# Kernel optimization log

Hardware: AMD Instinct MI355X
Metric: run time of the kernel (lower is better)

Reference implementation:

```python
import jax, jax.numpy as jnp
import numpy as np

B, N, C = 32, 1025, 768
H, D = 12, 64          # num_heads, head_dim
M = 4 * D              # num random features = 256
HEIGHT, WIDTH = 32, 32 # spatial grid; N = HEIGHT*WIDTH + 1 (CLS)
EPS = 1e-6


def setup_inputs() -> dict:
    key = jax.random.key(0)
    ks = jax.random.split(key, 7)
    x = jax.random.normal(ks[0], (B, N, C), jnp.float32)
    w_qkv = jax.random.normal(ks[1], (3 * C, C), jnp.float32) * 0.02
    w_proj = jax.random.normal(ks[2], (C, C), jnp.float32) * 0.02
    b_proj = jnp.zeros((C,), jnp.float32)
    c_row = jax.random.normal(ks[3], (H, D), jnp.float32) * 0.02
    c_col = jax.random.normal(ks[4], (H, D), jnp.float32) * 0.02
    # orthogonal random-feature projection (m, d): QR blocks scaled by chi norm
    blocks = []
    for i in range(M // D):
        Hm = jax.random.normal(jax.random.fold_in(ks[5], i), (D, D), jnp.float32)
        Q, _ = jnp.linalg.qr(Hm)
        nrm = jnp.linalg.norm(jax.random.normal(jax.random.fold_in(ks[6], i), (D,), jnp.float32))
        blocks.append(Q * nrm)
    proj_feat = jnp.concatenate(blocks, axis=0)  # (M, D)
    return {"x": x, "w_qkv": w_qkv, "w_proj": w_proj, "b_proj": b_proj,
            "c_row": c_row, "c_col": c_col, "proj_feat": proj_feat}


def _string(xp, c_row, c_col):
    """Circulant-STRING rotation. xp: (B,H,Np,D)."""
    rows = jnp.arange(HEIGHT, dtype=jnp.float32)
    cols = jnp.arange(WIDTH, dtype=jnp.float32)
    gr, gc = jnp.meshgrid(rows, cols, indexing='ij')
    pos_r = gr.ravel()  # (Np,)
    pos_c = gc.ravel()
    # g: (H, Np, D)
    g = pos_r[None, :, None] * c_row[:, None, :] + pos_c[None, :, None] * c_col[:, None, :]
    g_fft = jnp.fft.fft(g, axis=-1)
    exp_lambda = jnp.exp(2j * g_fft.imag)          # (H, Np, D) complex, unit modulus
    x_fft = jnp.fft.fft(xp, axis=-1)               # (B, H, Np, D) complex
    rotated = jnp.fft.ifft(exp_lambda[None] * x_fft, axis=-1).real
    return rotated.astype(xp.dtype)


def _favor(x, proj):
    """Positive random feature map. x: (B,H,N,D), proj: (M,D) -> (B,H,N,M)."""
    xs = x * (D ** -0.25)
    px = jnp.einsum('bhnd,md->bhnm', xs, proj)
    norm_sq = 0.5 * jnp.sum(xs * xs, axis=-1, keepdims=True)
    return jnp.exp(px - norm_sq)


def reference(x, w_qkv, w_proj, b_proj, c_row, c_col, proj_feat):
    qkv = x @ w_qkv.T                                  # (B, N, 3C)
    qkv = qkv.reshape(B, N, 3, H, D).transpose(2, 0, 3, 1, 4)  # (3,B,H,N,D)
    q, k, v = qkv[0], qkv[1], qkv[2]
    # N == HEIGHT*WIDTH + 1 -> CLS token at position 0 is left unrotated
    q_cls, q_p = q[:, :, :1, :], q[:, :, 1:, :]
    k_cls, k_p = k[:, :, :1, :], k[:, :, 1:, :]
    q = jnp.concatenate([q_cls, _string(q_p, c_row, c_col)], axis=2)
    k = jnp.concatenate([k_cls, _string(k_p, c_row, c_col)], axis=2)
    q_feat = _favor(q, proj_feat)                      # (B,H,N,M)
    k_feat = _favor(k, proj_feat)
    # bidirectional linear attention
    context = jnp.einsum('bhnm,bhne->bhme', k_feat, v) # (B,H,M,D)
    num = jnp.einsum('bhnm,bhme->bhne', q_feat, context)
    k_sum = k_feat.sum(axis=2)                         # (B,H,M)
    den = jnp.einsum('bhnm,bhm->bhn', q_feat, k_sum)[..., None]
    den = jnp.maximum(den, EPS)
    out = num / den                                    # (B,H,N,D)
    out = out.transpose(0, 2, 1, 3).reshape(B, N, C)
    return out @ w_proj.T + b_proj
```

## Files before the change

### kernel.cpp

```cpp
#include <hip/hip_runtime.h>
#include <math.h>

typedef _Float16 f16;
typedef _Float16 f16x8 __attribute__((ext_vector_type(8)));
typedef _Float16 f16x4 __attribute__((ext_vector_type(4)));
typedef float f32x4 __attribute__((ext_vector_type(4)));

#define LDSK 40
#define NTOK 1025
#define CC 768
#define HH 12
#define DD 64
#define MM 256
#define VPAD 1056
#define BN_ROWS 32800

__device__ __forceinline__ void load_row16(const f16* p, f16x8& a0, f16x8& a1) {
    a0 = *(const f16x8*)p;
    a1 = *(const f16x8*)(p + 8);
}
__device__ __forceinline__ void load_row16(const float* p, f16x8& a0, f16x8& a1) {
    const float4* q = (const float4*)p;
    float4 u0 = q[0], u1 = q[1], u2 = q[2], u3 = q[3];
    a0[0] = (f16)u0.x; a0[1] = (f16)u0.y; a0[2] = (f16)u0.z; a0[3] = (f16)u0.w;
    a0[4] = (f16)u1.x; a0[5] = (f16)u1.y; a0[6] = (f16)u1.z; a0[7] = (f16)u1.w;
    a1[0] = (f16)u2.x; a1[1] = (f16)u2.y; a1[2] = (f16)u2.z; a1[3] = (f16)u2.w;
    a1[4] = (f16)u3.x; a1[5] = (f16)u3.y; a1[6] = (f16)u3.z; a1[7] = (f16)u3.w;
}

__device__ __forceinline__ void gload16(const f16* g, f16* l) {
    __builtin_amdgcn_global_load_lds(
        (const __attribute__((address_space(1))) unsigned int*)g,
        (__attribute__((address_space(3))) unsigned int*)l, 16, 0, 0);
}

__global__ void k_diag(float* out, float v) {
    if (threadIdx.x == 0 && blockIdx.x == 0) out[0] = v;
}

__global__ __launch_bounds__(256) void k_cvt_x(const float* __restrict__ x, f16* __restrict__ xw) {
    size_t i = ((size_t)blockIdx.x * 256 + threadIdx.x) * 4;
    float4 v;
    if (i < (size_t)BN_ROWS * CC) v = *(const float4*)(x + i);
    else v = make_float4(0.f, 0.f, 0.f, 0.f);
    f16x4 o; o[0] = (f16)v.x; o[1] = (f16)v.y; o[2] = (f16)v.z; o[3] = (f16)v.w;
    *(f16x4*)(xw + i) = o;
}

__global__ __launch_bounds__(256) void k_cvt(const float* __restrict__ in, f16* __restrict__ out,
                                             long n, float scale) {
    long i = (long)blockIdx.x * 256 + threadIdx.x;
    if (i < n) out[i] = (f16)(in[i] * scale);
}

__global__ __launch_bounds__(256) void k_zpad(f16* __restrict__ v16t) {
    int bh = blockIdx.x;
    for (int u = threadIdx.x; u < 64 * 31; u += 256) {
        int d = u / 31, j = u - d * 31;
        v16t[((size_t)bh * DD + d) * VPAD + 1025 + j] = (f16)0.f;
    }
}

__global__ __launch_bounds__(64) void k_ab(const float* __restrict__ c_row,
                                           const float* __restrict__ c_col,
                                           float* __restrict__ ab) {
    int h = blockIdx.x, k = threadIdx.x;
    float sa = 0.f, sb = 0.f;
    for (int d = 0; d < 64; ++d) {
        float s = sinf((float)((k * d) & 63) * (6.283185307179586f / 64.f));
        sa += c_row[h * 64 + d] * s;
        sb += c_col[h * 64 + d] * s;
    }
    ab[h * 64 + k] = -2.f * sa;
    ab[768 + h * 64 + k] = -2.f * sb;
}

__global__ __launch_bounds__(64) void k_wcirc(const float* __restrict__ ab, float* __restrict__ wc) {
    int hp = blockIdx.x; int h = hp >> 10; int p = hp & 1023;
    float pr = (float)(p >> 5), pc = (float)(p & 31);
    int t = threadIdx.x;
    __shared__ float th[64];
    th[t] = pr * ab[h * 64 + t] + pc * ab[768 + h * 64 + t];
    __syncthreads();
    float s = 0.f;
    #pragma unroll 8
    for (int k = 0; k < 64; ++k) {
        float arg = th[k] + (float)((k * t) & 63) * (6.283185307179586f / 64.f);
        s += __cosf(arg);
    }
    wc[(size_t)hp * 64 + t] = s * (1.f / 64.f);
}

template <bool GA, typename TA, typename TB>
__device__ __forceinline__ void gemm128_core(const TA* __restrict__ A, const TB* __restrict__ Bm,
                                             int K, int row0, int col0, int Alim,
                                             f32x4 (&acc)[4][4],
                                             f16 (*As)[LDSK], f16 (*Bs)[LDSK]) {
    const int tid = threadIdx.x;
    const int lane = tid & 63;
    const int lr = tid >> 1, lk = (tid & 1) * 16;
    const int frow = lane & 15, fk = (lane >> 4) * 8;
    const int wave = tid >> 6, wr = wave >> 1, wc = wave & 1;
    for (int kt = 0; kt < K; kt += 32) {
        f16x8 a0 = {}, a1 = {}, b0, b1;
        if (!GA || (row0 + lr) < Alim)
            load_row16(A + (size_t)(row0 + lr) * K + kt + lk, a0, a1);
        load_row16(Bm + (size_t)(col0 + lr) * K + kt + lk, b0, b1);
        __syncthreads();
        *(f16x8*)&As[lr][lk] = a0; *(f16x8*)&As[lr][lk + 8] = a1;
        *(f16x8*)&Bs[lr][lk] = b0; *(f16x8*)&Bs[lr][lk + 8] = b1;
        __syncthreads();
        f16x8 af[4], bf[4];
        #pragma unroll
        for (int m = 0; m < 4; ++m) af[m] = *(const f16x8*)&As[wr * 64 + m * 16 + frow][fk];
        #pragma unroll
        for (int n = 0; n < 4; ++n) bf[n] = *(const f16x8*)&Bs[wc * 64 + n * 16 + frow][fk];
        #pragma unroll
        for (int m = 0; m < 4; ++m)
            #pragma unroll
            for (int n = 0; n < 4; ++n)
                acc[m][n] = __builtin_amdgcn_mfma_f32_16x16x32_f16(af[m], bf[n], acc[m][n], 0, 0, 0);
    }
}

__device__ __forceinline__ void gemm256_pipe(const f16* __restrict__ A, const f16* __restrict__ Bm,
                                             int row0, int col0, int aclamp,
                                             f32x4 (&acc)[8][4], f16* As, f16* Bs) {
    const int tid = threadIdx.x;
    const int lane = tid & 63, w = tid >> 6;
    const int frow = lane & 15;
    const int srow = lane >> 3;
    const int schk = ((lane & 7) ^ srow) * 8;
    const f16* aG[4]; const f16* bG[4];
    f16* aL[4]; f16* bL[4];
    #pragma unroll
    for (int j = 0; j < 4; ++j) {
        int ra = row0 + w * 32 + 8 * j + srow;
        if (ra > aclamp) ra = aclamp;
        aG[j] = A + (size_t)ra * CC + schk;
        bG[j] = Bm + (size_t)(col0 + w * 32 + 8 * j + srow) * CC + schk;
        aL[j] = As + (w * 32 + 8 * j) * 64;
        bL[j] = Bs + (w * 32 + 8 * j) * 64;
    }
    auto STAGE = [&](int tt) {
        int bo = (tt & 1) * 16384, ko = tt * 64;
        #pragma unroll
        for (int j = 0; j < 4; ++j) {
            gload16(aG[j] + ko, aL[j] + bo);
            gload16(bG[j] + ko, bL[j] + bo);
        }
    };
    STAGE(0);
    const int wr = w >> 2, wcn = w & 3;
    const int fk8 = (lane >> 4) * 8;
    const int cswz = (frow & 7) * 8;
    for (int t = 0; t < 12; ++t) {
        asm volatile("s_waitcnt vmcnt(0)" ::: "memory");
        __builtin_amdgcn_s_barrier();
        __builtin_amdgcn_sched_barrier(0);
        if (t < 11) STAGE(t + 1);
        const f16* Ac = As + (t & 1) * 16384;
        const f16* Bc = Bs + (t & 1) * 16384;
        #pragma unroll
        for (int ks = 0; ks < 2; ++ks) {
            const int co = (ks * 32 + fk8) ^ cswz;
            f16x8 af[8], bf[4];
            #pragma unroll
            for (int n = 0; n < 4; ++n)
                bf[n] = *(const f16x8*)&Bc[(wcn * 64 + n * 16 + frow) * 64 + co];
            #pragma unroll
            for (int m = 0; m < 8; ++m)
                af[m] = *(const f16x8*)&Ac[(wr * 128 + m * 16 + frow) * 64 + co];
            #pragma unroll
            for (int n = 0; n < 4; ++n)
                #pragma unroll
                for (int m = 0; m < 8; ++m)
                    acc[m][n] = __builtin_amdgcn_mfma_f32_16x16x32_f16(af[m], bf[n], acc[m][n], 0, 0, 0);
        }
    }
}

__global__ __launch_bounds__(512, 2) void k_gemm_qkv_256(const f16* __restrict__ A, const f16* __restrict__ Bm,
                                                         f16* __restrict__ q16, f16* __restrict__ k16,
                                                         f16* __restrict__ v16t) {
    __shared__ __attribute__((aligned(16))) f16 As[2 * 256 * 64];
    __shared__ __attribute__((aligned(16))) f16 Bs[2 * 256 * 64];
    const int q = 145, r = 1;
    int xg = blockIdx.x & 7, o8 = blockIdx.x >> 3;
    int wg = (xg < r ? xg * (q + 1) : r * (q + 1) + (xg - r) * q) + o8;
    int row0 = (wg / 9) * 256, col0 = (wg % 9) * 256;
    f32x4 acc[8][4] = {};
    gemm256_pipe(A, Bm, row0, col0, 32895, acc, As, Bs);
    const int lane = threadIdx.x & 63, w = threadIdx.x >> 6;
    const int wr = w >> 2, wcn = w & 3;
    int cb = col0 + wcn * 64 + (lane & 15);
    int tt = cb / CC;
    int h = (cb - tt * CC) >> 6;
    int d0 = lane & 15;
    int rb = row0 + wr * 128 + 4 * (lane >> 4);
    #pragma unroll
    for (int m = 0; m < 8; ++m)
        #pragma unroll
        for (int i = 0; i < 4; ++i) {
            int rr = rb + m * 16 + i;
            if (rr >= BN_ROWS) continue;
            int b = rr / NTOK, nn = rr - b * NTOK;
            size_t bh = (size_t)b * HH + h;
            if (tt == 0) {
                f16* p = q16 + (bh * NTOK + nn) * DD + d0;
                #pragma unroll
                for (int n = 0; n < 4; ++n) p[n * 16] = (f16)acc[m][n][i];
            } else if (tt == 1) {
                f16* p = k16 + (bh * NTOK + nn) * DD + d0;
                #pragma unroll
                for (int n = 0; n < 4; ++n) p[n * 16] = (f16)acc[m][n][i];
            } else {
                f16* p = v16t + (bh * DD + d0) * VPAD + nn;
                #pragma unroll
                for (int n = 0; n < 4; ++n) p[(size_t)n * 16 * VPAD] = (f16)acc[m][n][i];
            }
        }
}

__global__ __launch_bounds__(512, 2) void k_gemm_proj_256(const f16* __restrict__ A, const f16* __restrict__ Bm,
                                                          const float* __restrict__ bias, float* __restrict__ out) {
    __shared__ __attribute__((aligned(16))) f16 As[2 * 256 * 64];
    __shared__ __attribute__((aligned(16))) f16 Bs[2 * 256 * 64];
    const int q = 48, r = 3;
    int xg = blockIdx.x & 7, o8 = blockIdx.x >> 3;
    int wg = (xg < r ? xg * (q + 1) : r * (q + 1) + (xg - r) * q) + o8;
    int row0 = (wg / 3) * 256, col0 = (wg % 3) * 256;
    f32x4 acc[8][4] = {};
    gemm256_pipe(A, Bm, row0, col0, 32799, acc, As, Bs);
    const int lane = threadIdx.x & 63, w = threadIdx.x >> 6;
    const int wr = w >> 2, wcn = w & 3;
    int cb = col0 + wcn * 64 + (lane & 15);
    float bj[4];
    #pragma unroll
    for (int n = 0; n < 4; ++n) bj[n] = bias[cb + n * 16];
    int rb = row0 + wr * 128 + 4 * (lane >> 4);
    #pragma unroll
    for (int m = 0; m < 8; ++m)
        #pragma unroll
        for (int i = 0; i < 4; ++i) {
            int rr = rb + m * 16 + i;
            if (rr >= BN_ROWS) continue;
            float* p = out + (size_t)rr * CC + cb;
            #pragma unroll
            for (int n = 0; n < 4; ++n) p[n * 16] = acc[m][n][i] + bj[n];
        }
}

__device__ __forceinline__ void qkv_epilogue(f32x4 (&acc)[4][4], int row0, int col0,
                                             f16* __restrict__ q16, f16* __restrict__ k16,
                                             f16* __restrict__ v16t) {
    int lane = threadIdx.x & 63, wave = threadIdx.x >> 6;
    int wr = wave >> 1, wc = wave & 1;
    int rb = row0 + wr * 64 + 4 * (lane >> 4);
    int cb = col0 + wc * 64 + (lane & 15);
    #pragma unroll
    for (int m = 0; m < 4; ++m)
        #pragma unroll
        for (int n = 0; n < 4; ++n)
            #pragma unroll
            for (int i = 0; i < 4; ++i) {
                int r = rb + m * 16 + i;
                if (r >= BN_ROWS) continue;
                int j = cb + n * 16;
                int b = r / NTOK, nn = r - b * NTOK;
                int t = j / CC, rem = j - t * CC;
                int h = rem >> 6, d = rem & 63;
                size_t bh = (size_t)b * HH + h;
                f16 val = (f16)acc[m][n][i];
                if (t == 0) q16[(bh * NTOK + nn) * DD + d] = val;
                else if (t == 1) k16[(bh * NTOK + nn) * DD + d] = val;
                else v16t[(bh * DD + d) * VPAD + nn] = val;
            }
}

__global__ __launch_bounds__(256) void k_gemm_qkv_f32(const float* __restrict__ A, const f16* __restrict__ Bm,
                                                      f16* __restrict__ q16, f16* __restrict__ k16,
                                                      f16* __restrict__ v16t) {
    __shared__ __attribute__((aligned(16))) f16 As[128][LDSK];
    __shared__ __attribute__((aligned(16))) f16 Bs[128][LDSK];
    f32x4 acc[4][4] = {};
    int row0 = blockIdx.x * 128, col0 = blockIdx.y * 128;
    gemm128_core<true>(A, Bm, CC, row0, col0, BN_ROWS, acc, As, Bs);
    qkv_epilogue(acc, row0, col0, q16, k16, v16t);
}

__global__ __launch_bounds__(256) void k_rotate(const float* __restrict__ wcirc,
                                                f16* __restrict__ q16, f16* __restrict__ k16,
                                                float* __restrict__ nsqq, float* __restrict__ nsqk) {
    const int p = blockIdx.x, h = blockIdx.y;
    const int nn = p + 1;
    const int tid = threadIdx.x;
    __shared__ float wl[64];
    __shared__ __attribute__((aligned(16))) f16 Ws[64][72];
    __shared__ __attribute__((aligned(16))) f16 Xs[64][72];
    if (tid < 64) wl[tid] = wcirc[((size_t)h * 1024 + p) * 64 + tid];
    {
        const int row = tid >> 2;
        const int ch = (tid & 3) * 16;
        const int b = row & 31;
        const f16* src = ((row < 32) ? q16 : k16) + (((size_t)b * HH + h) * NTOK + nn) * DD + ch;
        f16x8 v0 = *(const f16x8*)src;
        f16x8 v1 = *(const f16x8*)(src + 8);
        *(f16x8*)&Xs[row][ch] = v0;
        *(f16x8*)&Xs[row][ch + 8] = v1;
    }
    __syncthreads();
    #pragma unroll
    for (int j = 0; j < 16; ++j) {
        int idx = tid * 16 + j;
        int d = idx >> 6, m = idx & 63;
        Ws[d][m] = (f16)wl[(d - m) & 63];
    }
    __syncthreads();
    const int lane = tid & 63, wave = tid >> 6;
    const int frow = lane & 15, fk = (lane >> 4) * 8;
    f32x4 acc[4] = {};
    #pragma unroll
    for (int kt = 0; kt < 64; kt += 32) {
        f16x8 a = *(const f16x8*)&Xs[wave * 16 + frow][kt + fk];
        #pragma unroll
        for (int n = 0; n < 4; ++n) {
            f16x8 bfr = *(const f16x8*)&Ws[n * 16 + frow][kt + fk];
            acc[n] = __builtin_amdgcn_mfma_f32_16x16x32_f16(a, bfr, acc[n], 0, 0, 0);
        }
    }
    #pragma unroll
    for (int i = 0; i < 4; ++i) {
        int row = wave * 16 + 4 * (lane >> 4) + i;
        int b = row & 31;
        f16* dst = ((row < 32) ? q16 : k16) + (((size_t)b * HH + h) * NTOK + nn) * DD;
        float ss = 0.f;
        #pragma unroll
        for (int n = 0; n < 4; ++n) {
            float v = acc[n][i];
            dst[n * 16 + (lane & 15)] = (f16)v;
            ss += v * v;
        }
        ss += __shfl_xor(ss, 1); ss += __shfl_xor(ss, 2);
        ss += __shfl_xor(ss, 4); ss += __shfl_xor(ss, 8);
        if ((lane & 15) == 0) {
            float* nd = (row < 32) ? nsqq : nsqk;
            nd[((size_t)b * HH + h) * NTOK + nn] = ss * (1.f / 16.f);
        }
    }
}

__global__ __launch_bounds__(256) void k_cls_nsq(const f16* __restrict__ q16, const f16* __restrict__ k16,
                                                 float* __restrict__ nsqq, float* __restrict__ nsqk) {
    int gw = (blockIdx.x * 256 + threadIdx.x) >> 6;
    int lane = threadIdx.x & 63;
    int which = gw & 1; int bh = gw >> 1;
    const f16* src = (which ? k16 : q16) + (size_t)bh * NTOK * DD;
    float v = (float)src[lane];
    float ss = v * v;
    for (int off = 1; off < 64; off <<= 1) ss += __shfl_xor(ss, off);
    if (lane == 0) (which ? nsqk : nsqq)[(size_t)bh * NTOK] = ss * (1.f / 16.f);
}

__global__ __launch_bounds__(512) void k_fctx(const f16* __restrict__ k16, const f16* __restrict__ v16t,
                                              const f16* __restrict__ pfeat, const float* __restrict__ nsqk,
                                              f16* __restrict__ ctxT) {
    __shared__ __attribute__((aligned(16))) f16 uLDS[80 * 136];
    f16 (*fts)[LDSK] = (f16(*)[LDSK])uLDS;
    f16 (*cx)[136]   = (f16(*)[136])uLDS;
    const int bh = blockIdx.x;
    const int tid = threadIdx.x;
    const int lane = tid & 63, w = tid >> 6;
    const int frow = lane & 15, fk8 = (lane >> 4) * 8;
    const int m0 = w * 32;
    f16x8 pf[2][2];
    #pragma unroll
    for (int mf = 0; mf < 2; ++mf)
        #pragma unroll
        for (int kf = 0; kf < 2; ++kf)
            pf[mf][kf] = *(const f16x8*)&pfeat[(m0 + mf * 16 + frow) * DD + kf * 32 + fk8];
    const f16* kb_base = k16 + (size_t)bh * NTOK * DD;
    const f16* vb_base = v16t + (size_t)bh * DD * VPAD;
    const float* ns_base = nsqk + (size_t)bh * NTOK;
    auto loadK = [&](f16x8 (&kb)[2][2], int n0) {
        #pragma unroll
        for (int nf = 0; nf < 2; ++nf) {
            int n = n0 + nf * 16 + frow;
            #pragma unroll
            for (int kf = 0; kf < 2; ++kf) {
                f16x8 z = {};
                if (n < NTOK) z = *(const f16x8*)&kb_base[(size_t)n * DD + kf * 32 + fk8];
                kb[nf][kf] = z;
            }
        }
    };
    f32x4 acc[2][5] = {};
    f16x8 kb[2][2];
    loadK(kb, 0);
    for (int n0 = 0; n0 < VPAD; n0 += 32) {
        f16x8 vb[4];
        #pragma unroll
        for (int ef = 0; ef < 4; ++ef)
            vb[ef] = *(const f16x8*)&vb_base[(size_t)(ef * 16 + frow) * VPAD + n0 + fk8];
        f32x4 fa[2][2] = {};
        #pragma unroll
        for (int kf = 0; kf < 2; ++kf)
            #pragma unroll
            for (int mf = 0; mf < 2; ++mf)
                #pragma unroll
                for (int nf = 0; nf < 2; ++nf)
                    fa[mf][nf] = __builtin_amdgcn_mfma_f32_16x16x32_f16(pf[mf][kf], kb[nf][kf], fa[mf][nf], 0, 0, 0);
        f16x8 kbn[2][2];
        loadK(kbn, n0 + 32);
        #pragma unroll
        for (int nf = 0; nf < 2; ++nf) {
            int ncol = n0 + nf * 16 + frow;
            float ns = (ncol < NTOK) ? ns_base[ncol] : 0.f;
            #pragma unroll
            for (int mf = 0; mf < 2; ++mf)
                #pragma unroll
                for (int i = 0; i < 4; ++i) {
                    int mloc = m0 + mf * 16 + 4 * (lane >> 4) + i;
                    float v = (ncol < NTOK) ? fminf(__expf(fa[mf][nf][i] - ns), 60000.f) : 0.f;
                    fts[mloc][nf * 16 + frow] = (f16)v;
                }
        }
        __syncthreads();
        f16x8 afr[2];
        #pragma unroll
        for (int mf = 0; mf < 2; ++mf) afr[mf] = *(const f16x8*)&fts[m0 + mf * 16 + frow][fk8];
        #pragma unroll
        for (int ef = 0; ef < 4; ++ef)
            #pragma unroll
            for (int mf = 0; mf < 2; ++mf)
                acc[mf][ef] = __builtin_amdgcn_mfma_f32_16x16x32_f16(afr[mf], vb[ef], acc[mf][ef], 0, 0, 0);
        {
            f16x8 bfr;
            #pragma unroll
            for (int j = 0; j < 8; ++j)
                bfr[j] = (f16)((frow == 0 && (n0 + fk8 + j) < NTOK) ? 1.f : 0.f);
            #pragma unroll
            for (int mf = 0; mf < 2; ++mf)
                acc[mf][4] = __builtin_amdgcn_mfma_f32_16x16x32_f16(afr[mf], bfr, acc[mf][4], 0, 0, 0);
        }
        __syncthreads();
        #pragma unroll
        for (int nf = 0; nf < 2; ++nf)
            #pragma unroll
            for (int kf = 0; kf < 2; ++kf)
                kb[nf][kf] = kbn[nf][kf];
    }
    #pragma unroll
    for (int p = 0; p < 2; ++p) {
        __syncthreads();
        if ((w >> 2) == p) {
            int mb = m0 - p * 128;
            #pragma unroll
            for (int mf = 0; mf < 2; ++mf)
                #pragma unroll
                for (int ef = 0; ef < 5; ++ef) {
                    int e = ef * 16 + frow;
                    f16x4 pk;
                    #pragma unroll
                    for (int i = 0; i < 4; ++i) pk[i] = (f16)acc[mf][ef][i];
                    *(f16x4*)&cx[e][mb + mf * 16 + 4 * (lane >> 4)] = pk;
                }
        }
        __syncthreads();
        for (int u = tid; u < 80 * 16; u += 512) {
            int e = u >> 4, seg = u & 15;
            *(f16x8*)&ctxT[((size_t)bh * 80 + e) * MM + p * 128 + seg * 8] =
                *(const f16x8*)&cx[e][seg * 8];
        }
    }
}

__global__ __launch_bounds__(256) void k_fnum(const f16* __restrict__ q16, const f16* __restrict__ pfeat,
                                              const float* __restrict__ nsqq, const f16* __restrict__ ctxT,
                                              f16* __restrict__ attn) {
    __shared__ __attribute__((aligned(16))) f16 qf_s[128][72];
    const int bh = blockIdx.y;
    const int b = bh / HH, h = bh - b * HH;
    const int t0 = blockIdx.x * 128;
    const int tid = threadIdx.x;
    const int lane = tid & 63, w = tid >> 6;
    const int frow = lane & 15, fk8 = (lane >> 4) * 8;
    const f16* qbase = q16 + (size_t)bh * NTOK * DD;
    const f16* cbase = ctxT + (size_t)bh * 80 * MM;
    f16x8 qa[2][2];
    float ns[2][4];
    #pragma unroll
    for (int tf = 0; tf < 2; ++tf) {
        int t = t0 + w * 32 + tf * 16 + frow;
        #pragma unroll
        for (int kf = 0; kf < 2; ++kf) {
            f16x8 z = {};
            if (t < NTOK) z = *(const f16x8*)&qbase[(size_t)t * DD + kf * 32 + fk8];
            qa[tf][kf] = z;
        }
        #pragma unroll
        for (int i = 0; i < 4; ++i) {
            int tr = t0 + w * 32 + tf * 16 + 4 * (lane >> 4) + i;
            ns[tf][i] = (tr < NTOK) ? nsqq[(size_t)bh * NTOK + tr] : 0.f;
        }
    }
    auto loadPB = [&](f16x8 (&pb)[2][2], int mc) {
        #pragma unroll
        for (int nf = 0; nf < 2; ++nf)
            #pragma unroll
            for (int kf = 0; kf < 2; ++kf)
                pb[nf][kf] = *(const f16x8*)&pfeat[(mc * 32 + nf * 16 + frow) * DD + kf * 32 + fk8];
    };
    f32x4 acc[2][5] = {};
    f16x8 pb[2][2];
    loadPB(pb, 0);
    #pragma unroll
    for (int mc = 0; mc < 8; ++mc) {
        f32x4 fa[2][2] = {};
        #pragma unroll
        for (int kf = 0; kf < 2; ++kf)
            #pragma unroll
            for (int tf = 0; tf < 2; ++tf)
                #pragma unroll
                for (int nf = 0; nf < 2; ++nf)
                    fa[tf][nf] = __builtin_amdgcn_mfma_f32_16x16x32_f16(qa[tf][kf], pb[nf][kf], fa[tf][nf], 0, 0, 0);
        f16x8 pbn[2][2];
        loadPB(pbn, (mc + 1) & 7);
        #pragma unroll
        for (int tf = 0; tf < 2; ++tf)
            #pragma unroll
            for (int nf = 0; nf < 2; ++nf)
                #pragma unroll
                for (int i = 0; i < 4; ++i) {
                    int tl = w * 32 + tf * 16 + 4 * (lane >> 4) + i;
                    float v = fminf(__expf(fa[tf][nf][i] - ns[tf][i]), 60000.f);
                    qf_s[tl][nf * 16 + frow] = (f16)v;
                }
        __syncthreads();
        f16x8 afr[2];
        #pragma unroll
        for (int tf = 0; tf < 2; ++tf) afr[tf] = *(const f16x8*)&qf_s[w * 32 + tf * 16 + frow][fk8];
        #pragma unroll
        for (int ef = 0; ef < 5; ++ef) {
            f16x8 bfr = *(const f16x8*)&cbase[(size_t)(ef * 16 + frow) * MM + mc * 32 + fk8];
            #pragma unroll
            for (int tf = 0; tf < 2; ++tf)
                acc[tf][ef] = __builtin_amdgcn_mfma_f32_16x16x32_f16(afr[tf], bfr, acc[tf][ef], 0, 0, 0);
        }
        __syncthreads();
        #pragma unroll
        for (int nf = 0; nf < 2; ++nf)
            #pragma unroll
            for (int kf = 0; kf < 2; ++kf)
                pb[nf][kf] = pbn[nf][kf];
    }
    #pragma unroll
    for (int tf = 0; tf < 2; ++tf)
        #pragma unroll
        for (int i = 0; i < 4; ++i) {
            float den = fmaxf(__shfl(acc[tf][4][i], lane & 48), 1e-6f);
            int tl = w * 32 + tf * 16 + 4 * (lane >> 4) + i;
            #pragma unroll
            for (int ef = 0; ef < 4; ++ef)
                qf_s[tl][ef * 16 + frow] = (f16)(acc[tf][ef][i] / den);
        }
    __syncthreads();
    for (int u = tid; u < 128 * 8; u += 256) {
        int tok = u >> 3, seg = u & 7;
        if (t0 + tok < NTOK)
            *(f16x8*)&attn[((size_t)(b * NTOK + t0 + tok)) * CC + h * DD + seg * 8] =
                *(const f16x8*)&qf_s[tok][seg * 8];
    }
}

__device__ __forceinline__ void proj_epilogue(f32x4 (&acc)[4][4], int row0, int col0,
                                              const float* __restrict__ bias, float* __restrict__ out) {
    int lane = threadIdx.x & 63, wave = threadIdx.x >> 6;
    int wr = wave >> 1, wc = wave & 1;
    int rb = row0 + wr * 64 + 4 * (lane >> 4);
    int cb = col0 + wc * 64 + (lane & 15);
    #pragma unroll
    for (int n = 0; n < 4; ++n) {
        int j = cb + n * 16;
        float bj = bias[j];
        #pragma unroll
        for (int m = 0; m < 4; ++m)
            #pragma unroll
            for (int i = 0; i < 4; ++i) {
                int r = rb + m * 16 + i;
                if (r < BN_ROWS) out[(size_t)r * CC + j] = acc[m][n][i] + bj;
            }
    }
}

__global__ __launch_bounds__(256) void k_gemm_proj(const f16* __restrict__ A, const f16* __restrict__ Bm,
                                                   const float* __restrict__ bias, float* __restrict__ out) {
    __shared__ __attribute__((aligned(16))) f16 As[128][LDSK];
    __shared__ __attribute__((aligned(16))) f16 Bs[128][LDSK];
    f32x4 acc[4][4] = {};
    int row0 = blockIdx.x * 128, col0 = blockIdx.y * 128;
    gemm128_core<true>(A, Bm, CC, row0, col0, BN_ROWS, acc, As, Bs);
    proj_epilogue(acc, row0, col0, bias, out);
}

extern "C" void kernel_launch(void* const* d_in, const int* in_sizes, int n_in,
                              void* d_out, int out_size, void* d_ws, size_t ws_size,
                              hipStream_t stream) {
    const float* x = (const float*)d_in[0];
    const float* w_qkv = (const float*)d_in[1];
    const float* w_proj = (const float*)d_in[2];
    const float* b_proj = (const float*)d_in[3];
    const float* c_row = (const float*)d_in[4];
    const float* c_col = (const float*)d_in[5];
    const float* proj_feat = (const float*)d_in[6];
    float* out = (float*)d_out;
    char* ws = (char*)d_ws;
    char* ob = (char*)d_out;

    const size_t O_WQKV  = 0;
    const size_t O_WPROJ = 3538944;
    const size_t O_Q16   = 4718592;
    const size_t O_K16   = 55099392;
    const size_t O_XW    = 105480192;
    const size_t NEED_B  = 105480192;
    const size_t NEED_A  = 156008448;
    if (ws_size < NEED_B) {
        k_diag<<<1, 64, 0, stream>>>(out, (float)((double)ws_size / 1048576.0));
        return;
    }
    const bool useA = (ws_size >= NEED_A);

    const size_t OD_V    = 0;
    const size_t OD_CTX  = 51904512;
    const size_t OD_WC   = 67633152;
    const size_t OD_NSQQ = 70778880;
    const size_t OD_NSQK = 72353280;
    const size_t OD_PF   = 73927680;
    const size_t OD_AB   = 73960448;

    f16* wqkv16  = (f16*)(ws + O_WQKV);
    f16* wproj16 = (f16*)(ws + O_WPROJ);
    f16* q16     = (f16*)(ws + O_Q16);
    f16* k16     = (f16*)(ws + O_K16);
    f16* xw16    = (f16*)(ws + O_XW);
    f16* v16t    = (f16*)(ob + OD_V);
    f16* ctxT    = (f16*)(ob + OD_CTX);
    float* wcirc = (float*)(ob + OD_WC);
    float* nsqq  = (float*)(ob + OD_NSQQ);
    float* nsqk  = (float*)(ob + OD_NSQK);
    f16* pfeat16 = (f16*)(ob + OD_PF);
    float* ab    = (float*)(ob + OD_AB);
    f16* attn16  = k16;

    k_cvt<<<6912, 256, 0, stream>>>(w_qkv, wqkv16, 1769472L, 1.f);
    k_cvt<<<2304, 256, 0, stream>>>(w_proj, wproj16, 589824L, 1.f);
    k_cvt<<<64, 256, 0, stream>>>(proj_feat, pfeat16, 16384L, 0.3535533906f);
    k_ab<<<12, 64, 0, stream>>>(c_row, c_col, ab);
    k_wcirc<<<12288, 64, 0, stream>>>(ab, wcirc);

    if (useA) {
        k_cvt_x<<<24672, 256, 0, stream>>>(x, xw16);
        k_gemm_qkv_256<<<1161, 512, 0, stream>>>(xw16, wqkv16, q16, k16, v16t);
    } else {
        k_gemm_qkv_f32<<<dim3(257, 18), 256, 0, stream>>>(x, wqkv16, q16, k16, v16t);
    }
    k_zpad<<<384, 256, 0, stream>>>(v16t);

    k_rotate<<<dim3(1024, 12), 256, 0, stream>>>(wcirc, q16, k16, nsqq, nsqk);
    k_cls_nsq<<<192, 256, 0, stream>>>(q16, k16, nsqq, nsqk);

    k_fctx<<<384, 512, 0, stream>>>(k16, v16t, pfeat16, nsqk, ctxT);
    k_fnum<<<dim3(9, 384), 256, 0, stream>>>(q16, pfeat16, nsqq, ctxT, attn16);

    if (useA) {
        k_gemm_proj_256<<<387, 512, 0, stream>>>(attn16, wproj16, b_proj, out);
    } else {
        k_gemm_proj<<<dim3(257, 6), 256, 0, stream>>>(attn16, wproj16, b_proj, out);
    }

    (void)in_sizes; (void)n_in; (void)out_size;
}
```

Baseline: 644.7 us.

## Use triple-buffered K=32 LDS pipeline with prefetch depth two in 256x256 GEMMs

New measurement: 687.6 us. 6.6% more time.

```diff
diff --git a/kernel.cpp b/kernel.cpp
--- a/kernel.cpp
+++ b/kernel.cpp
@@ -123,74 +123,75 @@
     }
 }
 
-__device__ __forceinline__ void gemm256_pipe(const f16* __restrict__ A, const f16* __restrict__ Bm,
-                                             int row0, int col0, int aclamp,
-                                             f32x4 (&acc)[8][4], f16* As, f16* Bs) {
+__device__ __forceinline__ void gemm256_r3(const f16* __restrict__ A, const f16* __restrict__ Bm,
+                                           int row0, int col0, int aclamp,
+                                           f32x4 (&acc)[8][4], f16* As, f16* Bs) {
     const int tid = threadIdx.x;
     const int lane = tid & 63, w = tid >> 6;
     const int frow = lane & 15;
-    const int srow = lane >> 3;
-    const int schk = ((lane & 7) ^ srow) * 8;
-    const f16* aG[4]; const f16* bG[4];
-    f16* aL[4]; f16* bL[4];
-    #pragma unroll
-    for (int j = 0; j < 4; ++j) {
-        int ra = row0 + w * 32 + 8 * j + srow;
-        if (ra > aclamp) ra = aclamp;
-        aG[j] = A + (size_t)ra * CC + schk;
-        bG[j] = Bm + (size_t)(col0 + w * 32 + 8 * j + srow) * CC + schk;
-        aL[j] = As + (w * 32 + 8 * j) * 64;
-        bL[j] = Bs + (w * 32 + 8 * j) * 64;
-    }
+    const int Cs = (lane & 7) ^ (lane >> 3);
+    const int sr2 = 2 * (lane >> 3) + (Cs >> 2);
+    const int sc = (Cs & 3) * 8;
+    int ra0 = row0 + w * 32 + sr2;       if (ra0 > aclamp) ra0 = aclamp;
+    int ra1 = row0 + w * 32 + 16 + sr2;  if (ra1 > aclamp) ra1 = aclamp;
+    const f16* aG0 = A + (size_t)ra0 * CC + sc;
+    const f16* aG1 = A + (size_t)ra1 * CC + sc;
+    const f16* bG0 = Bm + (size_t)(col0 + w * 32 + sr2) * CC + sc;
+    const f16* bG1 = Bm + (size_t)(col0 + w * 32 + 16 + sr2) * CC + sc;
+    const int ldsO0 = (w * 16) * 64;
+    const int ldsO1 = (w * 16 + 8) * 64;
     auto STAGE = [&](int tt) {
-        int bo = (tt & 1) * 16384, ko = tt * 64;
-        #pragma unroll
-        for (int j = 0; j < 4; ++j) {
-            gload16(aG[j] + ko, aL[j] + bo);
-            gload16(bG[j] + ko, bL[j] + bo);
+        const int so = (tt % 3) * 8192;
+        const int ko = tt * 32;
+        gload16(aG0 + ko, As + so + ldsO0);
+        gload16(aG1 + ko, As + so + ldsO1);
+        gload16(bG0 + ko, Bs + so + ldsO0);
+        gload16(bG1 + ko, Bs + so + ldsO1);
+    };
+    const int wr = w >> 2, wcn = w & 3;
+    const int phys = ((4 * (frow & 1)) | (lane >> 4)) ^ (frow >> 1);
+    const int cA = (wr * 64 + (frow >> 1)) * 64 + phys * 8;
+    const int cB = (wcn * 32 + (frow >> 1)) * 64 + phys * 8;
+    auto COMPUTE = [&](int kt) {
+        const f16* Ac = As + (kt % 3) * 8192;
+        const f16* Bc = Bs + (kt % 3) * 8192;
+        f16x8 bf[4];
+        #pragma unroll
+        for (int n = 0; n < 4; ++n) bf[n] = *(const f16x8*)&Bc[cB + n * 512];
+        #pragma unroll
+        for (int m = 0; m < 8; ++m) {
+            f16x8 af = *(const f16x8*)&Ac[cA + m * 512];
+            #pragma unroll
+            for (int n = 0; n < 4; ++n)
+                acc[m][n] = __builtin_amdgcn_mfma_f32_16x16x32_f16(af, bf[n], acc[m][n], 0, 0, 0);
         }
     };
     STAGE(0);
-    const int wr = w >> 2, wcn = w & 3;
-    const int fk8 = (lane >> 4) * 8;
-    const int cswz = (frow & 7) * 8;
-    for (int t = 0; t < 12; ++t) {
-        asm volatile("s_waitcnt vmcnt(0)" ::: "memory");
+    STAGE(1);
+    for (int kt = 0; kt < 23; ++kt) {
+        asm volatile("s_waitcnt vmcnt(4)" ::: "memory");
         __builtin_amdgcn_s_barrier();
         __builtin_amdgcn_sched_barrier(0);
-        if (t < 11) STAGE(t + 1);
-        const f16* Ac = As + (t & 1) * 16384;
-        const f16* Bc = Bs + (t & 1) * 16384;
-        #pragma unroll
-        for (int ks = 0; ks < 2; ++ks) {
-            const int co = (ks * 32 + fk8) ^ cswz;
-            f16x8 af[8], bf[4];
-            #pragma unroll
-            for (int n = 0; n < 4; ++n)
-                bf[n] = *(const f16x8*)&Bc[(wcn * 64 + n * 16 + frow) * 64 + co];
-            #pragma unroll
-            for (int m = 0; m < 8; ++m)
-                af[m] = *(const f16x8*)&Ac[(wr * 128 + m * 16 + frow) * 64 + co];
-            #pragma unroll
-            for (int n = 0; n < 4; ++n)
-                #pragma unroll
-                for (int m = 0; m < 8; ++m)
-                    acc[m][n] = __builtin_amdgcn_mfma_f32_16x16x32_f16(af[m], bf[n], acc[m][n], 0, 0, 0);
-        }
-    }
+        if (kt < 22) STAGE(kt + 2);
+        COMPUTE(kt);
+    }
+    asm volatile("s_waitcnt vmcnt(0)" ::: "memory");
+    __builtin_amdgcn_s_barrier();
+    __builtin_amdgcn_sched_barrier(0);
+    COMPUTE(23);
 }
 
 __global__ __launch_bounds__(512, 2) void k_gemm_qkv_256(const f16* __restrict__ A, const f16* __restrict__ Bm,
                                                          f16* __restrict__ q16, f16* __restrict__ k16,
                                                          f16* __restrict__ v16t) {
-    __shared__ __attribute__((aligned(16))) f16 As[2 * 256 * 64];
-    __shared__ __attribute__((aligned(16))) f16 Bs[2 * 256 * 64];
+    __shared__ __attribute__((aligned(16))) f16 As[3 * 8192];
+    __shared__ __attribute__((aligned(16))) f16 Bs[3 * 8192];
     const int q = 145, r = 1;
     int xg = blockIdx.x & 7, o8 = blockIdx.x >> 3;
     int wg = (xg < r ? xg * (q + 1) : r * (q + 1) + (xg - r) * q) + o8;
     int row0 = (wg / 9) * 256, col0 = (wg % 9) * 256;
     f32x4 acc[8][4] = {};
-    gemm256_pipe(A, Bm, row0, col0, 32895, acc, As, Bs);
+    gemm256_r3(A, Bm, row0, col0, 32895, acc, As, Bs);
     const int lane = threadIdx.x & 63, w = threadIdx.x >> 6;
     const int wr = w >> 2, wcn = w & 3;
     int cb = col0 + wcn * 64 + (lane & 15);
@@ -224,14 +225,14 @@
 
 __global__ __launch_bounds__(512, 2) void k_gemm_proj_256(const f16* __restrict__ A, const f16* __restrict__ Bm,
                                                           const float* __restrict__ bias, float* __restrict__ out) {
-    __shared__ __attribute__((aligned(16))) f16 As[2 * 256 * 64];
-    __shared__ __attribute__((aligned(16))) f16 Bs[2 * 256 * 64];
+    __shared__ __attribute__((aligned(16))) f16 As[3 * 8192];
+    __shared__ __attribute__((aligned(16))) f16 Bs[3 * 8192];
     const int q = 48, r = 3;
     int xg = blockIdx.x & 7, o8 = blockIdx.x >> 3;
     int wg = (xg < r ? xg * (q + 1) : r * (q + 1) + (xg - r) * q) + o8;
     int row0 = (wg / 3) * 256, col0 = (wg % 3) * 256;
     f32x4 acc[8][4] = {};
-    gemm256_pipe(A, Bm, row0, col0, 32799, acc, As, Bs);
+    gemm256_r3(A, Bm, row0, col0, 32799, acc, As, Bs);
     const int lane = threadIdx.x & 63, w = threadIdx.x >> 6;
     const int wr = w >> 2, wcn = w & 3;
     int cb = col0 + wcn * 64 + (lane & 15);
```
